# Performance work log

Measured on AMD Instinct MI355X. Metric: run time of the kernel, lower is better.

## Reference

```python
import jax, jax.numpy as jnp
from jax import lax
import numpy as np

B = 8; T = 64000
NFFT = 1024; HOP = 256
SC = 20; KS = 1024; PAD = 512
HEADS = 8; GH = 64; GO = 32
SPEC_DIM = 32 * (NFFT // 4) // 2   # 4096
NODE_DIM = SC + SPEC_DIM           # 4116
EPS = 1e-5
NEG_SLOPE = 0.2


def setup_inputs() -> dict:
    ks = jax.random.split(jax.random.key(0), 12)
    f32 = jnp.float32
    def rn(k, shp, s):
        return jax.random.normal(k, shp, dtype=f32) * s
    return {
        "x": jax.random.normal(ks[0], (B, 1, T), dtype=f32),
        "sinc_w": rn(ks[1], (SC, 1, KS), 0.03),
        "conv1_w": rn(ks[2], (32, 1, 3, 3), 0.1),
        "conv1_b": jnp.zeros((32,), f32),
        "bn1_g": jnp.ones((32,), f32),
        "bn1_b": jnp.zeros((32,), f32),
        "conv2_w": rn(ks[3], (32, 32, 3, 3), 0.06),
        "conv2_b": jnp.zeros((32,), f32),
        "bn2_g": jnp.ones((32,), f32),
        "bn2_b": jnp.zeros((32,), f32),
        "gat1_W": rn(ks[4], (NODE_DIM, HEADS * GH), 0.015),
        "gat1_asrc": rn(ks[5], (HEADS, GH), 0.1),
        "gat1_adst": rn(ks[6], (HEADS, GH), 0.1),
        "gat1_bias": jnp.zeros((HEADS * GH,), f32),
        "gat2_W": rn(ks[7], (HEADS * GH, GO), 0.04),
        "gat2_asrc": rn(ks[8], (1, GO), 0.1),
        "gat2_adst": rn(ks[9], (1, GO), 0.1),
        "gat2_bias": jnp.zeros((GO,), f32),
        "fc1_w": rn(ks[10], (GO, 128), 0.15),
        "fc1_b": jnp.zeros((128,), f32),
        "bnf_g": jnp.ones((128,), f32),
        "bnf_b": jnp.zeros((128,), f32),
        "fc2_w": rn(ks[11], (128, 2), 0.08),
        "fc2_b": jnp.zeros((2,), f32),
    }


def _bn2d_eval(z, g, b):
    # eval-mode BatchNorm2d with running_mean=0, running_var=1
    s = g / jnp.sqrt(1.0 + EPS)
    return z * s[None, :, None, None] + b[None, :, None, None]


def _conv2d(z, w, b):
    y = lax.conv_general_dilated(z, w, (1, 1), ((1, 1), (1, 1)),
                                 dimension_numbers=("NCHW", "OIHW", "NCHW"))
    return y + b[None, :, None, None]


def _gat_dense(hin, W, asrc, adst, bias, heads, fo, concat):
    # PyG GATConv on a fully-connected graph (add_self_loops=True default
    # => every node attends to all nodes including itself). Eval mode (no dropout).
    b, n, d = hin.shape
    h = jnp.einsum("bnd,dhf->bnhf", hin, W.reshape(d, heads, fo))
    s_src = jnp.einsum("bnhf,hf->bnh", h, asrc)   # alpha_j contribution
    s_dst = jnp.einsum("bnhf,hf->bnh", h, adst)   # alpha_i contribution
    e = jax.nn.leaky_relu(s_dst[:, :, None, :] + s_src[:, None, :, :], NEG_SLOPE)  # (b,i,j,h)
    a = jax.nn.softmax(e, axis=2)                 # softmax over sources j per dest i
    out = jnp.einsum("bijh,bjhf->bihf", a, h)
    out = out.reshape(b, n, heads * fo) if concat else out.mean(axis=2)
    return out + bias


def reference(x, sinc_w, conv1_w, conv1_b, bn1_g, bn1_b, conv2_w, conv2_b,
              bn2_g, bn2_b, gat1_W, gat1_asrc, gat1_adst, gat1_bias,
              gat2_W, gat2_asrc, gat2_adst, gat2_bias,
              fc1_w, fc1_b, bnf_g, bnf_b, fc2_w, fc2_b):
    b = x.shape[0]
    # --- sinc (band-pass) conv branch: conv1d k=1024, pad=512 ---
    sinc = lax.conv_general_dilated(x, sinc_w, (1,), ((PAD, PAD),),
                                    dimension_numbers=("NCH", "OIH", "NCH"))  # (b,20,T+1)
    Ls = (sinc.shape[-1] // 4) * 4
    sinc_feat = sinc[:, :, :Ls].reshape(b, SC, Ls // 4, 4).mean(-1)  # avg_pool1d(4)
    sinc_feat = jnp.transpose(sinc_feat, (0, 2, 1))                  # (b, Ls//4, 20)

    # --- STFT branch (torch.stft: center=True, reflect pad, rect window) ---
    xw = x[:, 0, :]
    xp = jnp.pad(xw, ((0, 0), (NFFT // 2, NFFT // 2)), mode="reflect")
    n_frames = 1 + T // HOP  # 251
    idx = np.arange(n_frames)[:, None] * HOP + np.arange(NFFT)
    frames = xp[:, idx]                                   # (b, 251, 1024)
    mag = jnp.abs(jnp.fft.rfft(frames, axis=-1))          # (b, 251, 513)
    logmag = jnp.log(mag + 1e-9)
    s = jnp.transpose(logmag, (0, 2, 1))[:, None]         # (b, 1, 513, 251)

    h = jax.nn.relu(_bn2d_eval(_conv2d(s, conv1_w, conv1_b), bn1_g, bn1_b))
    h = jax.nn.relu(_bn2d_eval(_conv2d(h, conv2_w, conv2_b), bn2_g, bn2_b))
    Fq = (h.shape[2] // 2) * 2
    Tt = (h.shape[3] // 2) * 2
    h = h[:, :, :Fq, :Tt].reshape(b, 32, Fq // 2, 2, Tt // 2, 2).max(axis=(3, 5))  # maxpool 2x2
    spec_feat = jnp.transpose(h, (0, 3, 1, 2)).reshape(b, -1, SPEC_DIM)  # (b, 250, 4096)

    n = min(sinc_feat.shape[1], spec_feat.shape[1])  # 250
    nodes = jnp.concatenate([sinc_feat[:, :n], spec_feat[:, :n]], axis=-1)  # (b,250,4116)

    g1 = jax.nn.relu(_gat_dense(nodes, gat1_W, gat1_asrc, gat1_adst, gat1_bias, HEADS, GH, True))
    g2 = _gat_dense(g1, gat2_W, gat2_asrc, gat2_adst, gat2_bias, 1, GO, False)
    emb = g2.mean(axis=1)  # (b, 32) graph-mean readout

    z = emb @ fc1_w + fc1_b
    z = jax.nn.relu(z * (bnf_g / jnp.sqrt(1.0 + EPS)) + bnf_b)  # eval BN1d
    out = z @ fc2_w + fc2_b
    return (out, emb)
```

## Files before the change

### kernel.cpp

```cpp
#include <hip/hip_runtime.h>
#include <hip/hip_bf16.h>
#include <math.h>

#define TB 8
#define TT 64000
#define NFRAMES 251
#define NROWS (TB*NFRAMES)
#define GROWS 2048
#define NBINS 513
#define NBPAD 576
#define NNODE 250
#define NODE_DIM 4116
#define KPAD 4128

typedef __attribute__((ext_vector_type(8))) short short8;
typedef __attribute__((ext_vector_type(4))) float floatx4;

static __device__ __forceinline__ unsigned short f2bf(float x) {
    __hip_bfloat16 h = __float2bfloat16(x);
    return *(unsigned short*)&h;
}
static __device__ __forceinline__ float bf2f(unsigned short u) {
    __hip_bfloat16 h = *(__hip_bfloat16*)&u;
    return __bfloat162float(h);
}

__global__ __launch_bounds__(256) void k_prep(
    const float* __restrict__ x, const float* __restrict__ sinc_w,
    const float* __restrict__ c2w, const float* __restrict__ g2bn,
    const float* __restrict__ c1w, const float* __restrict__ g1bn,
    const float* __restrict__ W,
    unsigned short* __restrict__ fh, unsigned short* __restrict__ fl,
    unsigned short* __restrict__ bch, unsigned short* __restrict__ bcl,
    unsigned short* __restrict__ bsh, unsigned short* __restrict__ bsl,
    unsigned short* __restrict__ wbt, unsigned short* __restrict__ Bp,
    unsigned short* __restrict__ Bc1,
    unsigned short* __restrict__ Wt, unsigned short* __restrict__ nodesb,
    unsigned short* __restrict__ h1t, unsigned short* __restrict__ h2t) {
    __shared__ unsigned short tile[64][65];
    int bi = blockIdx.x, tid = threadIdx.x;
    if (bi < 2048) {
        int idx = bi * 256 + tid;
        int row = idx >> 8, r = idx & 255;
        int b = row >> 8, j = row & 255;
        int u = j * 256 + r - 512;
        if (u < 0) u = -u;
        if (u >= TT) u = 2 * TT - 2 - u;
        float v = x[b * TT + u];
        unsigned short h = f2bf(v);
        fh[idx] = h;
        fl[idx] = f2bf(v - bf2f(h));
    } else if (bi < 2624) {
        int idx = (bi - 2048) * 256 + tid;
        int k = idx >> 8, r = idx & 255;
        float s = 0.f, c = 0.f;
        if (k < NBINS) {
            int mm = (k * r) & 1023;
            sincospif((float)mm * (1.0f / 512.0f), &s, &c);
        }
        unsigned short chv = f2bf(c), shv = f2bf(s);
        bch[idx] = chv; bcl[idx] = f2bf(c - bf2f(chv));
        bsh[idx] = shv; bsl[idx] = f2bf(s - bf2f(shv));
    } else if (bi < 3144) {
        int local = bi - 2624;
        int kt = local % 65, nt = local / 65;
        for (int idx = tid; idx < 4096; idx += 256) {
            int r = idx >> 6, c = idx & 63;
            int kp = kt * 64 + r;
            int k;
            if (kp < 20) k = kp;
            else if (kp < NODE_DIM) { int t = kp - 20; k = 20 + (t & 15) * 256 + (t >> 4); }
            else k = -1;
            float v = (k >= 0) ? W[k * 512 + nt * 64 + c] : 0.f;
            tile[r][c] = f2bf(v);
        }
        __syncthreads();
        for (int idx = tid; idx < 4096; idx += 256) {
            int nl = idx >> 6, kl = idx & 63;
            int k = kt * 64 + kl;
            if (k < KPAD)
                Wt[(size_t)(nt * 64 + nl) * KPAD + k] = tile[kl][nl];
        }
    } else if (bi < 3276) {
        int idx = (bi - 3144) * 256 + tid;
        if (idx < 32 * 1056) {
            int c = idx / 1056, m = idx - c * 1056;
            float s = 0.f;
            if (c < 20 && m < 1027) {
                #pragma unroll
                for (int d = 0; d < 4; d++) {
                    int k = m - d;
                    if (k >= 0 && k < 1024) s += sinc_w[c * 1024 + k];
                }
                s *= 0.25f;
            }
            wbt[idx] = f2bf(s);
        }
    } else if (bi < 3312) {
        int idx = (bi - 3276) * 256 + tid;
        if (idx < 9216) {
            int j = idx & 7, lane = (idx >> 3) & 63, ct = (idx >> 9) & 1, s = idx >> 10;
            int co = ct * 16 + (lane & 15);
            int ci = (lane >> 4) * 8 + j;
            float inv = rsqrtf(1.0f + 1e-5f);
            Bp[idx] = f2bf(c2w[co * 288 + ci * 9 + s] * (g2bn[co] * inv));
        }
    } else if (bi < 3508) {
        int idx = (bi - 3312) * 256 + tid;
        if (idx < 24000) {
            int row = idx / 12, c = idx - row * 12;
            nodesb[(size_t)row * KPAD + 4116 + c] = 0;
        } else if (idx < 48576) {
            int t = idx - 24000; int r = t / 6, c = t - r * 6;
            h1t[(size_t)r * 256 + 250 + c] = 0;
        } else if (idx < 50112) {
            int t = idx - 48576; int r = t / 6, c = t - r * 6;
            h2t[(size_t)r * 256 + 250 + c] = 0;
        }
    } else {
        int idx = (bi - 3508) * 256 + tid;
        if (idx < 1024) {
            int ch = idx >> 5, k = idx & 31;
            float inv = rsqrtf(1.0f + 1e-5f);
            int t; int typ;
            if (k < 8)       { t = k;      typ = 0; }
            else if (k < 16) { t = k - 8;  typ = 0; }
            else if (k < 24) { t = k - 16; typ = 1; }
            else if (k == 24 || k == 25) { t = 8; typ = 0; }
            else if (k == 26) { t = 8; typ = 1; }
            else { t = 0; typ = 2; }
            unsigned short outv = 0;
            if (typ != 2) {
                float wv = c1w[ch * 9 + t] * (g1bn[ch] * inv);
                unsigned short whi = f2bf(wv);
                outv = (typ == 0) ? whi : f2bf(wv - bf2f(whi));
            }
            Bc1[idx] = outv;
        }
    }
}

__global__ __launch_bounds__(256) void k_dftsinc(const unsigned short* __restrict__ fh,
                                                 const unsigned short* __restrict__ fl,
                                                 const unsigned short* __restrict__ ch,
                                                 const unsigned short* __restrict__ cl,
                                                 const unsigned short* __restrict__ sh,
                                                 const unsigned short* __restrict__ sl,
                                                 float* __restrict__ GTR,
                                                 float* __restrict__ GTI,
                                                 const float* __restrict__ x,
                                                 const unsigned short* __restrict__ wbt,
                                                 unsigned short* __restrict__ nodesb) {
    __shared__ __align__(16) unsigned char smem[34048];
    int tid = threadIdx.x;
    int bi = blockIdx.x;
    if (bi >= 576) {
        unsigned short* xs = (unsigned short*)smem;
        int local = bi - 576;
        int ut = local & 3, b = local >> 2;
        int base = 256 * ut - 512;
        for (int i = tid; i < 1312; i += 256) {
            int g = base + i;
            float v = (g >= 0 && g < TT) ? x[b * TT + g] : 0.f;
            xs[i] = f2bf(v);
        }
        __syncthreads();
        int w = tid >> 6, lane = tid & 63;
        int q = lane >> 4, col = lane & 15;
        floatx4 acc[2];
        acc[0] = acc[1] = (floatx4){0.f, 0.f, 0.f, 0.f};
        for (int K0 = 0; K0 < 1056; K0 += 32) {
            int off = 4 * (w * 16 + col) + K0 + q * 8;
            unsigned long long lo = *(const unsigned long long*)&xs[off];
            unsigned long long hi = *(const unsigned long long*)&xs[off + 4];
            union { unsigned long long u64[2]; short8 s8; } cv;
            cv.u64[0] = lo; cv.u64[1] = hi;
            short8 af = cv.s8;
            #pragma unroll
            for (int ni = 0; ni < 2; ni++) {
                short8 bf = *(const short8*)(wbt + (size_t)(ni * 16 + col) * 1056 + K0 + q * 8);
                acc[ni] = __builtin_amdgcn_mfma_f32_16x16x32_bf16(af, bf, acc[ni], 0, 0, 0);
            }
        }
        #pragma unroll
        for (int ni = 0; ni < 2; ni++)
            #pragma unroll
            for (int rr = 0; rr < 4; rr++) {
                int u = ut * 64 + w * 16 + q * 4 + rr;
                int c = ni * 16 + col;
                if (u < NNODE && c < 20)
                    nodesb[(size_t)(b * NNODE + u) * KPAD + c] = f2bf(acc[ni][rr]);
            }
        return;
    }
    unsigned short* Ah  = (unsigned short*)smem;
    unsigned short* Al  = (unsigned short*)(smem + 2560);
    unsigned short* Bch = (unsigned short*)(smem + 5120);
    unsigned short* Bcl = (unsigned short*)(smem + 10240);
    unsigned short* Bsh = (unsigned short*)(smem + 15360);
    unsigned short* Bsl = (unsigned short*)(smem + 20480);
    float* TR = (float*)(smem + 25600);
    int N0 = (bi % 9) * 64, M0 = (bi / 9) * 32;
    int br = tid >> 2, bc = (tid & 3) * 8;
    size_t boff = (size_t)(N0 + br) * 256 + bc;
    int ar = (tid & 127) >> 2, ac = (tid & 3) * 8;
    size_t aoff = (size_t)(M0 + ar) * 256 + ac;
    bool loA = tid < 128;
    int w = tid >> 6, lane = tid & 63;
    int q = lane >> 4, col = lane & 15;
    int mb = (w >> 1) * 16, nb = (w & 1) * 32;
    floatx4 aR[2], aI[2];
    aR[0] = aR[1] = aI[0] = aI[1] = (floatx4){0.f, 0.f, 0.f, 0.f};

    for (int K0 = 0; K0 < 256; K0 += 32) {
        if (loA) *(short8*)&Ah[ar * 40 + ac] = *(const short8*)(fh + aoff + K0);
        else     *(short8*)&Al[ar * 40 + ac] = *(const short8*)(fl + aoff + K0);
        *(short8*)&Bch[br * 40 + bc] = *(const short8*)(ch + boff + K0);
        *(short8*)&Bcl[br * 40 + bc] = *(const short8*)(cl + boff + K0);
        *(short8*)&Bsh[br * 40 + bc] = *(const short8*)(sh + boff + K0);
        *(short8*)&Bsl[br * 40 + bc] = *(const short8*)(sl + boff + K0);
        __syncthreads();
        short8 ahv = *(const short8*)&Ah[(mb + col) * 40 + q * 8];
        short8 alv = *(const short8*)&Al[(mb + col) * 40 + q * 8];
        #pragma unroll
        for (int ni = 0; ni < 2; ni++) {
            short8 chv = *(const short8*)&Bch[(nb + ni * 16 + col) * 40 + q * 8];
            short8 clv = *(const short8*)&Bcl[(nb + ni * 16 + col) * 40 + q * 8];
            short8 shv = *(const short8*)&Bsh[(nb + ni * 16 + col) * 40 + q * 8];
            short8 slv = *(const short8*)&Bsl[(nb + ni * 16 + col) * 40 + q * 8];
            aR[ni] = __builtin_amdgcn_mfma_f32_16x16x32_bf16(ahv, chv, aR[ni], 0, 0, 0);
            aR[ni] = __builtin_amdgcn_mfma_f32_16x16x32_bf16(ahv, clv, aR[ni], 0, 0, 0);
            aR[ni] = __builtin_amdgcn_mfma_f32_16x16x32_bf16(alv, chv, aR[ni], 0, 0, 0);
            aI[ni] = __builtin_amdgcn_mfma_f32_16x16x32_bf16(ahv, shv, aI[ni], 0, 0, 0);
            aI[ni] = __builtin_amdgcn_mfma_f32_16x16x32_bf16(ahv, slv, aI[ni], 0, 0, 0);
            aI[ni] = __builtin_amdgcn_mfma_f32_16x16x32_bf16(alv, shv, aI[ni], 0, 0, 0);
        }
        __syncthreads();
    }
    int bin_l = tid >> 2, ms = (tid & 3) * 8;
    #pragma unroll
    for (int ni = 0; ni < 2; ni++)
        #pragma unroll
        for (int rr = 0; rr < 4; rr++)
            TR[(nb + ni * 16 + col) * 33 + mb + q * 4 + rr] = aR[ni][rr];
    __syncthreads();
    {
        float* dst = GTR + (size_t)(N0 + bin_l) * 2048 + M0 + ms;
        #pragma unroll
        for (int j = 0; j < 8; j++) dst[j] = TR[bin_l * 33 + ms + j];
    }
    __syncthreads();
    #pragma unroll
    for (int ni = 0; ni < 2; ni++)
        #pragma unroll
        for (int rr = 0; rr < 4; rr++)
            TR[(nb + ni * 16 + col) * 33 + mb + q * 4 + rr] = aI[ni][rr];
    __syncthreads();
    {
        float* dst = GTI + (size_t)(N0 + bin_l) * 2048 + M0 + ms;
        #pragma unroll
        for (int j = 0; j < 8; j++) dst[j] = TR[bin_l * 33 + ms + j];
    }
}

#define O1STR 40
__global__ __launch_bounds__(256) void k_conv2f(const float* __restrict__ GTR,
                                                const float* __restrict__ GTI,
                                                const unsigned short* __restrict__ Bc1,
                                                const float* __restrict__ c1b,
                                                const float* __restrict__ g1bn,
                                                const float* __restrict__ b1bn,
                                                const unsigned short* __restrict__ Bp,
                                                const float* __restrict__ c2b,
                                                const float* __restrict__ g2bn,
                                                const float* __restrict__ b2bn,
                                                unsigned short* __restrict__ nodesb) {
    __shared__ __align__(16) unsigned short o1s[18 * 18 * O1STR];
    __shared__ float S0s[20][20];
    __shared__ float b1s[32];
    __shared__ float b2s[32];
    int tid = threadIdx.x;
    int b = blockIdx.z;
    int F0 = blockIdx.y * 8;
    int T0 = blockIdx.x * 8;
    float inv = rsqrtf(1.0f + 1e-5f);
    if (tid < 32) {
        b1s[tid] = c1b[tid] * (g1bn[tid] * inv) + b1bn[tid];
        b2s[tid] = c2b[tid] * (g2bn[tid] * inv) + b2bn[tid];
    }
    for (int i = tid; i < 400; i += 256) {
        int r = i / 20, c = i - r * 20;
        int bin = 2 * F0 - 2 + r, fr = 2 * T0 - 2 + c;
        float v = 0.f;
        if (bin >= 0 && bin < 513 && fr >= 0 && fr < 251) {
            size_t base = (size_t)bin * 2048 + b * 256 + fr;
            float gr0 = GTR[base], gr1 = GTR[base + 1], gr2 = GTR[base + 2], gr3 = GTR[base + 3];
            float gs0 = GTI[base], gs1 = GTI[base + 1], gs2 = GTI[base + 2], gs3 = GTI[base + 3];
            float fre, fim;
            switch (bin & 3) {
                case 0: fre = gr0 + gr1 + gr2 + gr3; fim = gs0 + gs1 + gs2 + gs3; break;
                case 1: fre = gr0 - gs1 - gr2 + gs3; fim = gs0 + gr1 - gs2 - gr3; break;
                case 2: fre = gr0 - gr1 + gr2 - gr3; fim = gs0 - gs1 + gs2 - gs3; break;
                default: fre = gr0 + gs1 - gr2 - gs3; fim = gs0 - gr1 - gs2 + gr3; break;
            }
            v = logf(sqrtf(fmaf(fre, fre, fim * fim)) + 1e-9f);
        }
        S0s[r][c] = v;
    }
    __syncthreads();

    int lane = tid & 63, w = tid >> 6;
    int q = lane >> 4, col = lane & 15;

    {
        short8 bfr0 = *(const short8*)(Bc1 + (size_t)col * 32 + q * 8);
        short8 bfr1 = *(const short8*)(Bc1 + (size_t)(16 + col) * 32 + q * 8);
        for (int mt = w; mt < 21; mt += 4) {
            int p = mt * 16 + col;
            int pc = p < 324 ? p : 0;
            int pr = (pc * 228) >> 12;
            int pt = pc - pr * 18;
            float tv[9];
            #pragma unroll
            for (int di = 0; di < 3; di++)
                #pragma unroll
                for (int dj = 0; dj < 3; dj++)
                    tv[di * 3 + dj] = S0s[pr + di][pt + dj];
            unsigned short hu[9], lu[9];
            #pragma unroll
            for (int i = 0; i < 9; i++) {
                hu[i] = f2bf(tv[i]);
                lu[i] = f2bf(tv[i] - bf2f(hu[i]));
            }
            short8 af;
            if (q == 1) {
                af[0] = lu[0]; af[1] = lu[1]; af[2] = lu[2]; af[3] = lu[3];
                af[4] = lu[4]; af[5] = lu[5]; af[6] = lu[6]; af[7] = lu[7];
            } else if (q == 3) {
                af[0] = hu[8]; af[1] = lu[8]; af[2] = hu[8]; af[3] = 0;
                af[4] = 0; af[5] = 0; af[6] = 0; af[7] = 0;
            } else {
                af[0] = hu[0]; af[1] = hu[1]; af[2] = hu[2]; af[3] = hu[3];
                af[4] = hu[4]; af[5] = hu[5]; af[6] = hu[6]; af[7] = hu[7];
            }
            floatx4 c0 = (floatx4){0.f, 0.f, 0.f, 0.f};
            floatx4 c1 = (floatx4){0.f, 0.f, 0.f, 0.f};
            c0 = __builtin_amdgcn_mfma_f32_16x16x32_bf16(af, bfr0, c0, 0, 0, 0);
            c1 = __builtin_amdgcn_mfma_f32_16x16x32_bf16(af, bfr1, c1, 0, 0, 0);
            #pragma unroll
            for (int rr2 = 0; rr2 < 4; rr2++) {
                int pp = mt * 16 + q * 4 + rr2;
                if (pp < 324) {
                    int qr = (pp * 228) >> 12, qt = pp - qr * 18;
                    int r1 = 2 * F0 - 1 + qr, t1 = 2 * T0 - 1 + qt;
                    bool valid = (r1 >= 0 && r1 < 513 && t1 >= 0 && t1 < 251);
                    float v0 = fmaxf(c0[rr2] + b1s[col], 0.f);
                    float v1 = fmaxf(c1[rr2] + b1s[16 + col], 0.f);
                    o1s[pp * O1STR + col]      = valid ? f2bf(v0) : (unsigned short)0;
                    o1s[pp * O1STR + 16 + col] = valid ? f2bf(v1) : (unsigned short)0;
                }
            }
        }
    }
    __syncthreads();

    floatx4 acc[4][2];
    #pragma unroll
    for (int rt = 0; rt < 4; rt++)
        #pragma unroll
        for (int ct = 0; ct < 2; ct++)
            acc[rt][ct] = (floatx4){0.f, 0.f, 0.f, 0.f};

    #pragma unroll
    for (int s = 0; s < 9; s++) {
        const int di = s / 3, dj = s % 3;
        short8 bf0 = *(const short8*)&Bp[(s * 2 + 0) * 512 + lane * 8];
        short8 bf1 = *(const short8*)&Bp[(s * 2 + 1) * 512 + lane * 8];
        #pragma unroll
        for (int rt = 0; rt < 4; rt++) {
            short8 af = *(const short8*)&o1s[((w * 4 + rt + di) * 18 + (col + dj)) * O1STR + q * 8];
            acc[rt][0] = __builtin_amdgcn_mfma_f32_16x16x32_bf16(af, bf0, acc[rt][0], 0, 0, 0);
            acc[rt][1] = __builtin_amdgcn_mfma_f32_16x16x32_bf16(af, bf1, acc[rt][1], 0, 0, 0);
        }
    }
    __syncthreads();

    unsigned short* nb = o1s;
    #pragma unroll
    for (int ct = 0; ct < 2; ct++) {
        float bb = b2s[ct * 16 + col];
        #pragma unroll
        for (int fp2 = 0; fp2 < 2; fp2++)
            #pragma unroll
            for (int tc2 = 0; tc2 < 2; tc2++) {
                float m0 = fmaxf(
                    fmaxf(acc[2 * fp2][ct][2 * tc2], acc[2 * fp2][ct][2 * tc2 + 1]),
                    fmaxf(acc[2 * fp2 + 1][ct][2 * tc2], acc[2 * fp2 + 1][ct][2 * tc2 + 1]));
                float v = fmaxf(m0 + bb, 0.f);
                int nl = (2 * q + tc2) * 2 + ct;
                int fl = 2 * w + fp2;
                nb[nl * 136 + fl * 16 + col] = f2bf(v);
            }
    }
    __syncthreads();

    int nl = tid >> 4, part = tid & 15;
    int node_g = 2 * T0 + nl;
    if (node_g < NNODE) {
        unsigned short* dst = nodesb + (size_t)(b * NNODE + node_g) * KPAD + 20 + F0 * 16 + part * 8;
        *(short8*)(dst) = *(const short8*)&nb[nl * 136 + part * 8];
    }
}

__global__ __launch_bounds__(256) void k_gat1s(const unsigned short* __restrict__ A,
                                               const unsigned short* __restrict__ Bt,
                                               float* __restrict__ hpart) {
    __shared__ __align__(16) unsigned short As[64 * 40];
    __shared__ __align__(16) unsigned short Bs[64 * 40];
    int tid = threadIdx.x;
    int N0 = blockIdx.x * 64, M0 = blockIdx.y * 64;
    int kc = blockIdx.z;
    int ks = (kc == 0) ? 0 : (33 + 32 * (kc - 1));
    int ke = 33 + 32 * kc;
    if (kc == 0) ke = 33;
    int sr = tid >> 2, sc = (tid & 3) * 8;
    int w = tid >> 6, lane = tid & 63;
    int q = lane >> 4, col = lane & 15;
    int mb = (w >> 1) * 32, nb = (w & 1) * 32;
    floatx4 acc[2][2];
    acc[0][0] = acc[0][1] = acc[1][0] = acc[1][1] = (floatx4){0.f, 0.f, 0.f, 0.f};
    short8 z8 = {0, 0, 0, 0, 0, 0, 0, 0};
    int mA = M0 + sr;
    bool mv = mA < 2000;
    const unsigned short* pa = A + (size_t)mA * KPAD + sc;
    const unsigned short* pb = Bt + (size_t)(N0 + sr) * KPAD + sc;

    for (int kk = ks; kk < ke; kk++) {
        int K0 = kk * 32;
        short8 va = mv ? *(const short8*)(pa + K0) : z8;
        short8 vb = *(const short8*)(pb + K0);
        *(short8*)&As[sr * 40 + sc] = va;
        *(short8*)&Bs[sr * 40 + sc] = vb;
        __syncthreads();
        short8 a0 = *(const short8*)&As[(mb + col) * 40 + q * 8];
        short8 a1 = *(const short8*)&As[(mb + 16 + col) * 40 + q * 8];
        short8 b0 = *(const short8*)&Bs[(nb + col) * 40 + q * 8];
        short8 b1 = *(const short8*)&Bs[(nb + 16 + col) * 40 + q * 8];
        acc[0][0] = __builtin_amdgcn_mfma_f32_16x16x32_bf16(a0, b0, acc[0][0], 0, 0, 0);
        acc[0][1] = __builtin_amdgcn_mfma_f32_16x16x32_bf16(a0, b1, acc[0][1], 0, 0, 0);
        acc[1][0] = __builtin_amdgcn_mfma_f32_16x16x32_bf16(a1, b0, acc[1][0], 0, 0, 0);
        acc[1][1] = __builtin_amdgcn_mfma_f32_16x16x32_bf16(a1, b1, acc[1][1], 0, 0, 0);
        __syncthreads();
    }
    float* out = hpart + (size_t)kc * 1024000;
    #pragma unroll
    for (int mi = 0; mi < 2; mi++)
        #pragma unroll
        for (int ni = 0; ni < 2; ni++)
            #pragma unroll
            for (int rr = 0; rr < 4; rr++) {
                int m = M0 + mb + mi * 16 + q * 4 + rr;
                if (m < 2000)
                    out[m * 512 + N0 + nb + ni * 16 + col] = acc[mi][ni][rr];
            }
}

__global__ __launch_bounds__(256) void k_hred(const float* __restrict__ hpart,
                                              const float* __restrict__ asrc,
                                              const float* __restrict__ adst,
                                              unsigned short* __restrict__ h1t,
                                              float* __restrict__ ssrc,
                                              float* __restrict__ sdst) {
    int m = blockIdx.x;
    int tid = threadIdx.x;
    int n1 = tid, n2 = tid + 256;
    size_t base = (size_t)m * 512;
    float s1 = hpart[base + n1] + hpart[base + n1 + 1024000] +
               hpart[base + n1 + 2048000] + hpart[base + n1 + 3072000];
    float s2 = hpart[base + n2] + hpart[base + n2 + 1024000] +
               hpart[base + n2 + 2048000] + hpart[base + n2 + 3072000];
    int bb = m / NNODE, j = m - bb * NNODE;
    int hh1 = n1 >> 6, f1 = n1 & 63;
    int hh2 = n2 >> 6, f2 = n2 & 63;
    h1t[((size_t)((bb * 8 + hh1) * 64 + f1)) * 256 + j] = f2bf(s1);
    h1t[((size_t)((bb * 8 + hh2) * 64 + f2)) * 256 + j] = f2bf(s2);
    float ps1 = s1 * asrc[n1], pd1 = s1 * adst[n1];
    float ps2 = s2 * asrc[n2], pd2 = s2 * adst[n2];
    for (int off = 32; off > 0; off >>= 1) {
        ps1 += __shfl_down(ps1, off); pd1 += __shfl_down(pd1, off);
        ps2 += __shfl_down(ps2, off); pd2 += __shfl_down(pd2, off);
    }
    int lane = tid & 63, w = tid >> 6;
    if (lane == 0) {
        ssrc[m * 8 + w] = ps1;     sdst[m * 8 + w] = pd1;
        ssrc[m * 8 + 4 + w] = ps2; sdst[m * 8 + 4 + w] = pd2;
    }
}

#define PSTR 264
__global__ __launch_bounds__(256) void k_att1(const float* __restrict__ ssrc,
                                              const float* __restrict__ sdst,
                                              const unsigned short* __restrict__ h1t,
                                              const float* __restrict__ bias,
                                              float* __restrict__ g1) {
    __shared__ __align__(16) unsigned short Ps[128 * PSTR];
    __shared__ float ss[NNODE];
    __shared__ float red[4];
    int mhalf = blockIdx.x, bh = blockIdx.y;
    int b = bh >> 3, h = bh & 7;
    int tid = threadIdx.x;
    for (int j = tid; j < NNODE; j += 256) ss[j] = ssrc[(b * NNODE + j) * 8 + h];
    __syncthreads();
    float mv = (tid < NNODE) ? ss[tid] : -1e30f;
    for (int off = 32; off > 0; off >>= 1) mv = fmaxf(mv, __shfl_down(mv, off));
    if ((tid & 63) == 0) red[tid >> 6] = mv;
    __syncthreads();
    float smaxv = fmaxf(fmaxf(red[0], red[1]), fmaxf(red[2], red[3]));
    if (tid < 128) {
        unsigned short* row = Ps + tid * PSTR;
        int row_g = mhalf * 128 + tid;
        short8 z8 = {0, 0, 0, 0, 0, 0, 0, 0};
        if (row_g >= NNODE) {
            #pragma unroll
            for (int j = 0; j < 256; j += 8) *(short8*)(row + j) = z8;
        } else {
            float d = sdst[(b * NNODE + row_g) * 8 + h];
            float e0 = d + smaxv;
            float mx = e0 > 0.f ? e0 : 0.2f * e0;
            float den = 0.f;
            for (int j = 0; j < NNODE; j++) {
                float e = d + ss[j];
                e = e > 0.f ? e : 0.2f * e;
                den += __expf(e - mx);
            }
            float rden = 1.f / den;
            for (int j0 = 0; j0 < 256; j0 += 8) {
                unsigned short wv[8];
                #pragma unroll
                for (int jj = 0; jj < 8; jj++) {
                    int j = j0 + jj;
                    float wt = 0.f;
                    if (j < NNODE) {
                        float e = d + ss[j];
                        e = e > 0.f ? e : 0.2f * e;
                        wt = __expf(e - mx) * rden;
                    }
                    wv[jj] = f2bf(wt);
                }
                *(short8*)(row + j0) = *(const short8*)wv;
            }
        }
    }
    __syncthreads();
    int w = tid >> 6, lane = tid & 63;
    int q = lane >> 4, col = lane & 15;
    const unsigned short* Hb = h1t + (size_t)bh * 16384;
    floatx4 acc[2][4];
    #pragma unroll
    for (int mi = 0; mi < 2; mi++)
        #pragma unroll
        for (int ni = 0; ni < 4; ni++)
            acc[mi][ni] = (floatx4){0.f, 0.f, 0.f, 0.f};
    for (int k0 = 0; k0 < 256; k0 += 32) {
        short8 af[2], bf[4];
        #pragma unroll
        for (int mi = 0; mi < 2; mi++)
            af[mi] = *(const short8*)&Ps[((w * 2 + mi) * 16 + col) * PSTR + k0 + q * 8];
        #pragma unroll
        for (int ni = 0; ni < 4; ni++)
            bf[ni] = *(const short8*)(Hb + (size_t)(ni * 16 + col) * 256 + k0 + q * 8);
        #pragma unroll
        for (int mi = 0; mi < 2; mi++)
            #pragma unroll
            for (int ni = 0; ni < 4; ni++)
                acc[mi][ni] = __builtin_amdgcn_mfma_f32_16x16x32_bf16(af[mi], bf[ni], acc[mi][ni], 0, 0, 0);
    }
    #pragma unroll
    for (int mi = 0; mi < 2; mi++)
        #pragma unroll
        for (int ni = 0; ni < 4; ni++)
            #pragma unroll
            for (int rr = 0; rr < 4; rr++) {
                int i = mhalf * 128 + (w * 2 + mi) * 16 + q * 4 + rr;
                int f = ni * 16 + col;
                if (i < NNODE)
                    g1[(b * NNODE + i) * 512 + h * 64 + f] =
                        fmaxf(acc[mi][ni][rr] + bias[h * 64 + f], 0.f);
            }
}

__global__ __launch_bounds__(256) void k_h2(const float* __restrict__ g1,
                                            const float* __restrict__ W2,
                                            const float* __restrict__ a2src,
                                            const float* __restrict__ a2dst,
                                            unsigned short* __restrict__ h2t,
                                            float* __restrict__ s2src,
                                            float* __restrict__ s2dst) {
    int row = blockIdx.x * 4 + (threadIdx.x >> 6);
    if (row >= 2000) return;
    int lane = threadIdx.x & 63;
    int o = lane & 31, half = lane >> 5;
    const float* gr = &g1[row * 512 + half * 256];
    float acc = 0.f;
    for (int k = 0; k < 256; k++) acc = fmaf(gr[k], W2[(half * 256 + k) * 32 + o], acc);
    acc += __shfl_down(acc, 32);
    float ps = acc * a2src[o], pd = acc * a2dst[o];
    for (int off = 16; off > 0; off >>= 1) {
        ps += __shfl_down(ps, off, 32);
        pd += __shfl_down(pd, off, 32);
    }
    if (lane == 0) { s2src[row] = ps; s2dst[row] = pd; }
    if (lane < 32) {
        int b = row / NNODE, j = row - b * NNODE;
        h2t[((size_t)(b * 32 + o)) * 256 + j] = f2bf(acc);
    }
}

__global__ __launch_bounds__(256) void k_att2(const float* __restrict__ s2src,
                                              const float* __restrict__ s2dst,
                                              const unsigned short* __restrict__ h2t,
                                              const float* __restrict__ bias2,
                                              float* __restrict__ g2) {
    __shared__ __align__(16) unsigned short Ps[256 * PSTR];
    __shared__ float ss[NNODE];
    __shared__ float red[4];
    int b = blockIdx.x;
    int tid = threadIdx.x;
    for (int j = tid; j < NNODE; j += 256) ss[j] = s2src[b * NNODE + j];
    __syncthreads();
    float mv = (tid < NNODE) ? ss[tid] : -1e30f;
    for (int off = 32; off > 0; off >>= 1) mv = fmaxf(mv, __shfl_down(mv, off));
    if ((tid & 63) == 0) red[tid >> 6] = mv;
    __syncthreads();
    float smaxv = fmaxf(fmaxf(red[0], red[1]), fmaxf(red[2], red[3]));
    {
        unsigned short* row = Ps + tid * PSTR;
        short8 z8 = {0, 0, 0, 0, 0, 0, 0, 0};
        if (tid >= NNODE) {
            #pragma unroll
            for (int j = 0; j < 256; j += 8) *(short8*)(row + j) = z8;
        } else {
            float d = s2dst[b * NNODE + tid];
            float e0 = d + smaxv;
            float mx = e0 > 0.f ? e0 : 0.2f * e0;
            float den = 0.f;
            for (int j = 0; j < NNODE; j++) {
                float e = d + ss[j];
                e = e > 0.f ? e : 0.2f * e;
                den += __expf(e - mx);
            }
            float rden = 1.f / den;
            for (int j0 = 0; j0 < 256; j0 += 8) {
                unsigned short wv[8];
                #pragma unroll
                for (int jj = 0; jj < 8; jj++) {
                    int j = j0 + jj;
                    float wt = 0.f;
                    if (j < NNODE) {
                        float e = d + ss[j];
                        e = e > 0.f ? e : 0.2f * e;
                        wt = __expf(e - mx) * rden;
                    }
                    wv[jj] = f2bf(wt);
                }
                *(short8*)(row + j0) = *(const short8*)wv;
            }
        }
    }
    __syncthreads();
    int w = tid >> 6, lane = tid & 63;
    int q = lane >> 4, col = lane & 15;
    const unsigned short* Hb = h2t + (size_t)b * 8192;
    floatx4 acc[4][2];
    #pragma unroll
    for (int mi = 0; mi < 4; mi++)
        #pragma unroll
        for (int ni = 0; ni < 2; ni++)
            acc[mi][ni] = (floatx4){0.f, 0.f, 0.f, 0.f};
    for (int k0 = 0; k0 < 256; k0 += 32) {
        short8 af[4], bf[2];
        #pragma unroll
        for (int mi = 0; mi < 4; mi++)
            af[mi] = *(const short8*)&Ps[((w * 4 + mi) * 16 + col) * PSTR + k0 + q * 8];
        #pragma unroll
        for (int ni = 0; ni < 2; ni++)
            bf[ni] = *(const short8*)(Hb + (size_t)(ni * 16 + col) * 256 + k0 + q * 8);
        #pragma unroll
        for (int mi = 0; mi < 4; mi++)
            #pragma unroll
            for (int ni = 0; ni < 2; ni++)
                acc[mi][ni] = __builtin_amdgcn_mfma_f32_16x16x32_bf16(af[mi], bf[ni], acc[mi][ni], 0, 0, 0);
    }
    #pragma unroll
    for (int mi = 0; mi < 4; mi++)
        #pragma unroll
        for (int ni = 0; ni < 2; ni++)
            #pragma unroll
            for (int rr = 0; rr < 4; rr++) {
                int i = (w * 4 + mi) * 16 + q * 4 + rr;
                int f = ni * 16 + col;
                if (i < NNODE)
                    g2[(b * NNODE + i) * 32 + f] = acc[mi][ni][rr] + bias2[f];
            }
}

__global__ __launch_bounds__(256) void k_fc(const float* __restrict__ g2,
                                            const float* __restrict__ fc1w,
                                            const float* __restrict__ fc1b,
                                            const float* __restrict__ bnfg,
                                            const float* __restrict__ bnfb,
                                            const float* __restrict__ fc2w,
                                            const float* __restrict__ fc2b,
                                            float* __restrict__ dout) {
    __shared__ float es[256];
    __shared__ float zs[1024];
    int tid = threadIdx.x;
    {
        int b = tid >> 5, f = tid & 31;
        float s = 0.f;
        #pragma unroll 5
        for (int i = 0; i < NNODE; i++) s += g2[((size_t)(b * NNODE + i)) * 32 + f];
        s *= (1.0f / 250.0f);
        es[tid] = s;
        dout[16 + tid] = s;
    }
    __syncthreads();
    float inv = rsqrtf(1.0f + 1e-5f);
    #pragma unroll
    for (int rep = 0; rep < 4; rep++) {
        int idx = tid + rep * 256;
        int b = idx >> 7, j = idx & 127;
        float a = fc1b[j];
        #pragma unroll
        for (int k = 0; k < 32; k++) a = fmaf(es[b * 32 + k], fc1w[k * 128 + j], a);
        a = a * (bnfg[j] * inv) + bnfb[j];
        zs[idx] = fmaxf(a, 0.f);
    }
    __syncthreads();
    if (tid < 16) {
        int b = tid >> 1, o = tid & 1;
        float a = fc2b[o];
        for (int k = 0; k < 128; k++) a = fmaf(zs[b * 128 + k], fc2w[k * 2 + o], a);
        dout[b * 2 + o] = a;
    }
}

extern "C" void kernel_launch(void* const* d_in, const int* in_sizes, int n_in,
                              void* d_out, int out_size, void* d_ws, size_t ws_size,
                              hipStream_t stream) {
    (void)in_sizes; (void)n_in; (void)out_size; (void)ws_size;
    const float* x       = (const float*)d_in[0];
    const float* sinc_w  = (const float*)d_in[1];
    const float* conv1_w = (const float*)d_in[2];
    const float* conv1_b = (const float*)d_in[3];
    const float* bn1_g   = (const float*)d_in[4];
    const float* bn1_b   = (const float*)d_in[5];
    const float* conv2_w = (const float*)d_in[6];
    const float* conv2_b = (const float*)d_in[7];
    const float* bn2_g   = (const float*)d_in[8];
    const float* bn2_b   = (const float*)d_in[9];
    const float* gat1_W  = (const float*)d_in[10];
    const float* gat1_as = (const float*)d_in[11];
    const float* gat1_ad = (const float*)d_in[12];
    const float* gat1_bi = (const float*)d_in[13];
    const float* gat2_W  = (const float*)d_in[14];
    const float* gat2_as = (const float*)d_in[15];
    const float* gat2_ad = (const float*)d_in[16];
    const float* gat2_bi = (const float*)d_in[17];
    const float* fc1_w   = (const float*)d_in[18];
    const float* fc1_b   = (const float*)d_in[19];
    const float* bnf_g   = (const float*)d_in[20];
    const float* bnf_b   = (const float*)d_in[21];
    const float* fc2_w   = (const float*)d_in[22];
    const float* fc2_b   = (const float*)d_in[23];
    float* dout = (float*)d_out;

    unsigned short* fh  = (unsigned short*)d_ws;
    unsigned short* fl  = fh + (size_t)GROWS * 256;
    unsigned short* bch = fl + (size_t)GROWS * 256;
    unsigned short* bcl = bch + (size_t)NBPAD * 256;
    unsigned short* bsh = bcl + (size_t)NBPAD * 256;
    unsigned short* bsl = bsh + (size_t)NBPAD * 256;
    float* GTR = (float*)(bsl + (size_t)NBPAD * 256);
    float* GTI = GTR + (size_t)GROWS * NBPAD;
    float* S0  = GTI + (size_t)GROWS * NBPAD;
    unsigned short* wbt = (unsigned short*)(S0 + 1030104);
    unsigned short* bpk = wbt + 32 * 1056;
    unsigned short* Bc1 = bpk + 9216;
    unsigned short* Wt  = Bc1 + 1024;
    unsigned short* nodesb = Wt + (size_t)512 * KPAD;
    unsigned short* Pn  = nodesb + (size_t)2000 * KPAD;
    unsigned short* h1t = Pn + (size_t)64 * 256 * 256;
    unsigned short* h2t = h1t + (size_t)64 * 64 * 256;
    unsigned short* P2n = h2t + (size_t)8 * 32 * 256;
    float* hpart = (float*)(P2n + (size_t)8 * 256 * 256);
    float* ssrc1 = hpart + 4 * 1024000;
    float* sdst1 = ssrc1 + 16000;
    float* g1    = sdst1 + 16000;
    float* s2src = g1 + 1024000;
    float* s2dst = s2src + 2000;
    float* g2    = s2dst + 2000;

    hipLaunchKernelGGL(k_prep, dim3(3512), dim3(256), 0, stream,
                       x, sinc_w, conv2_w, bn2_g, conv1_w, bn1_g, gat1_W,
                       fh, fl, bch, bcl, bsh, bsl, wbt, bpk, Bc1, Wt, nodesb, h1t, h2t);
    hipLaunchKernelGGL(k_dftsinc, dim3(608), dim3(256), 0, stream,
                       fh, fl, bch, bcl, bsh, bsl, GTR, GTI, x, wbt, nodesb);
    hipLaunchKernelGGL(k_conv2f, dim3(16, 32, 8), dim3(256), 0, stream,
                       GTR, GTI, Bc1, conv1_b, bn1_g, bn1_b, bpk, conv2_b, bn2_g, bn2_b, nodesb);
    hipLaunchKernelGGL(k_gat1s, dim3(8, 32, 4), dim3(256), 0, stream, nodesb, Wt, hpart);
    hipLaunchKernelGGL(k_hred, dim3(2000), dim3(256), 0, stream,
                       hpart, gat1_as, gat1_ad, h1t, ssrc1, sdst1);
    hipLaunchKernelGGL(k_att1, dim3(2, 64), dim3(256), 0, stream,
                       ssrc1, sdst1, h1t, gat1_bi, g1);
    hipLaunchKernelGGL(k_h2, dim3(500), dim3(256), 0, stream,
                       g1, gat2_W, gat2_as, gat2_ad, h2t, s2src, s2dst);
    hipLaunchKernelGGL(k_att2, dim3(8), dim3(256), 0, stream,
                       s2src, s2dst, h2t, gat2_bi, g2);
    hipLaunchKernelGGL(k_fc, dim3(1), dim3(256), 0, stream,
                       g2, fc1_w, fc1_b, bnf_g, bnf_b, fc2_w, fc2_b, dout);
}
```

Measured before the change: 313.2 us.

## Fuse split-K reduction into GAT1 attention and fold FC head into GAT2

Removes the k_hred kernel. Each k_att1 block now sums the four split-K partials for its batch/head slice, converts to bf16 into shared memory, and computes the source/destination attention scores in place. This drops the h1t and score round-trips through global memory. It also removes the k_fc launch: each k_att2 block reduces its graph mean in shared memory and runs the small FC head for its batch, cutting two launches. The cost is that each k_att1 block (two per batch-head) redundantly re-reduces the same partials, giving less parallelism than 2000 blocks for that reduction. Shared memory per block also grows.

```diff
diff --git a/kernel.cpp b/kernel.cpp
--- a/kernel.cpp
+++ b/kernel.cpp
@@ -36,7 +36,7 @@
     unsigned short* __restrict__ wbt, unsigned short* __restrict__ Bp,
     unsigned short* __restrict__ Bc1,
     unsigned short* __restrict__ Wt, unsigned short* __restrict__ nodesb,
-    unsigned short* __restrict__ h1t, unsigned short* __restrict__ h2t) {
+    unsigned short* __restrict__ h2t) {
     __shared__ unsigned short tile[64][65];
     int bi = blockIdx.x, tid = threadIdx.x;
     if (bi < 2048) {
@@ -110,11 +110,8 @@
         if (idx < 24000) {
             int row = idx / 12, c = idx - row * 12;
             nodesb[(size_t)row * KPAD + 4116 + c] = 0;
-        } else if (idx < 48576) {
+        } else if (idx < 25536) {
             int t = idx - 24000; int r = t / 6, c = t - r * 6;
-            h1t[(size_t)r * 256 + 250 + c] = 0;
-        } else if (idx < 50112) {
-            int t = idx - 48576; int r = t / 6, c = t - r * 6;
             h2t[(size_t)r * 256 + 250 + c] = 0;
         }
     } else {
@@ -465,53 +462,43 @@
             }
 }
 
-__global__ __launch_bounds__(256) void k_hred(const float* __restrict__ hpart,
+#define PSTR 264
+__global__ __launch_bounds__(256) void k_att1(const float* __restrict__ hpart,
                                               const float* __restrict__ asrc,
                                               const float* __restrict__ adst,
-                                              unsigned short* __restrict__ h1t,
-                                              float* __restrict__ ssrc,
-                                              float* __restrict__ sdst) {
-    int m = blockIdx.x;
-    int tid = threadIdx.x;
-    int n1 = tid, n2 = tid + 256;
-    size_t base = (size_t)m * 512;
-    float s1 = hpart[base + n1] + hpart[base + n1 + 1024000] +
-               hpart[base + n1 + 2048000] + hpart[base + n1 + 3072000];
-    float s2 = hpart[base + n2] + hpart[base + n2 + 1024000] +
-               hpart[base + n2 + 2048000] + hpart[base + n2 + 3072000];
-    int bb = m / NNODE, j = m - bb * NNODE;
-    int hh1 = n1 >> 6, f1 = n1 & 63;
-    int hh2 = n2 >> 6, f2 = n2 & 63;
-    h1t[((size_t)((bb * 8 + hh1) * 64 + f1)) * 256 + j] = f2bf(s1);
-    h1t[((size_t)((bb * 8 + hh2) * 64 + f2)) * 256 + j] = f2bf(s2);
-    float ps1 = s1 * asrc[n1], pd1 = s1 * adst[n1];
-    float ps2 = s2 * asrc[n2], pd2 = s2 * adst[n2];
-    for (int off = 32; off > 0; off >>= 1) {
-        ps1 += __shfl_down(ps1, off); pd1 += __shfl_down(pd1, off);
-        ps2 += __shfl_down(ps2, off); pd2 += __shfl_down(pd2, off);
-    }
-    int lane = tid & 63, w = tid >> 6;
-    if (lane == 0) {
-        ssrc[m * 8 + w] = ps1;     sdst[m * 8 + w] = pd1;
-        ssrc[m * 8 + 4 + w] = ps2; sdst[m * 8 + 4 + w] = pd2;
-    }
-}
-
-#define PSTR 264
-__global__ __launch_bounds__(256) void k_att1(const float* __restrict__ ssrc,
-                                              const float* __restrict__ sdst,
-                                              const unsigned short* __restrict__ h1t,
                                               const float* __restrict__ bias,
                                               float* __restrict__ g1) {
     __shared__ __align__(16) unsigned short Ps[128 * PSTR];
-    __shared__ float ss[NNODE];
+    __shared__ __align__(16) unsigned short hL[64 * PSTR];
+    __shared__ float ssA[NNODE];
+    __shared__ float sdA[NNODE];
     __shared__ float red[4];
     int mhalf = blockIdx.x, bh = blockIdx.y;
     int b = bh >> 3, h = bh & 7;
     int tid = threadIdx.x;
-    for (int j = tid; j < NNODE; j += 256) ss[j] = ssrc[(b * NNODE + j) * 8 + h];
-    __syncthreads();
-    float mv = (tid < NNODE) ? ss[tid] : -1e30f;
+    int lane = tid & 63, w = tid >> 6;
+    {
+        float av = asrc[h * 64 + lane];
+        float dv = adst[h * 64 + lane];
+        for (int j = w; j < 256; j += 4) {
+            if (j < NNODE) {
+                size_t base = ((size_t)(b * NNODE + j)) * 512 + h * 64 + lane;
+                float s = hpart[base] + hpart[base + 1024000] +
+                          hpart[base + 2048000] + hpart[base + 3072000];
+                hL[lane * PSTR + j] = f2bf(s);
+                float ps = s * av, pd = s * dv;
+                for (int off = 32; off > 0; off >>= 1) {
+                    ps += __shfl_down(ps, off);
+                    pd += __shfl_down(pd, off);
+                }
+                if (lane == 0) { ssA[j] = ps; sdA[j] = pd; }
+            } else {
+                hL[lane * PSTR + j] = 0;
+            }
+        }
+    }
+    __syncthreads();
+    float mv = (tid < NNODE) ? ssA[tid] : -1e30f;
     for (int off = 32; off > 0; off >>= 1) mv = fmaxf(mv, __shfl_down(mv, off));
     if ((tid & 63) == 0) red[tid >> 6] = mv;
     __syncthreads();
@@ -524,12 +511,12 @@
             #pragma unroll
             for (int j = 0; j < 256; j += 8) *(short8*)(row + j) = z8;
         } else {
-            float d = sdst[(b * NNODE + row_g) * 8 + h];
+            float d = sdA[row_g];
             float e0 = d + smaxv;
             float mx = e0 > 0.f ? e0 : 0.2f * e0;
             float den = 0.f;
             for (int j = 0; j < NNODE; j++) {
-                float e = d + ss[j];
+                float e = d + ssA[j];
                 e = e > 0.f ? e : 0.2f * e;
                 den += __expf(e - mx);
             }
@@ -541,7 +528,7 @@
                     int j = j0 + jj;
                     float wt = 0.f;
                     if (j < NNODE) {
-                        float e = d + ss[j];
+                        float e = d + ssA[j];
                         e = e > 0.f ? e : 0.2f * e;
                         wt = __expf(e - mx) * rden;
                     }
@@ -552,9 +539,7 @@
         }
     }
     __syncthreads();
-    int w = tid >> 6, lane = tid & 63;
     int q = lane >> 4, col = lane & 15;
-    const unsigned short* Hb = h1t + (size_t)bh * 16384;
     floatx4 acc[2][4];
     #pragma unroll
     for (int mi = 0; mi < 2; mi++)
@@ -568,7 +553,7 @@
             af[mi] = *(const short8*)&Ps[((w * 2 + mi) * 16 + col) * PSTR + k0 + q * 8];
         #pragma unroll
         for (int ni = 0; ni < 4; ni++)
-            bf[ni] = *(const short8*)(Hb + (size_t)(ni * 16 + col) * 256 + k0 + q * 8);
+            bf[ni] = *(const short8*)&hL[(ni * 16 + col) * PSTR + k0 + q * 8];
         #pragma unroll
         for (int mi = 0; mi < 2; mi++)
             #pragma unroll
@@ -620,10 +605,18 @@
                                               const float* __restrict__ s2dst,
                                               const unsigned short* __restrict__ h2t,
                                               const float* __restrict__ bias2,
-                                              float* __restrict__ g2) {
+                                              const float* __restrict__ fc1w,
+                                              const float* __restrict__ fc1b,
+                                              const float* __restrict__ bnfg,
+                                              const float* __restrict__ bnfb,
+                                              const float* __restrict__ fc2w,
+                                              const float* __restrict__ fc2b,
+                                              float* __restrict__ dout) {
     __shared__ __align__(16) unsigned short Ps[256 * PSTR];
     __shared__ float ss[NNODE];
     __shared__ float red[4];
+    __shared__ float es2[32];
+    __shared__ float zs2[128];
     int b = blockIdx.x;
     int tid = threadIdx.x;
     for (int j = tid; j < NNODE; j += 256) ss[j] = s2src[b * NNODE + j];
@@ -691,6 +684,8 @@
             for (int ni = 0; ni < 2; ni++)
                 acc[mi][ni] = __builtin_amdgcn_mfma_f32_16x16x32_bf16(af[mi], bf[ni], acc[mi][ni], 0, 0, 0);
     }
+    __syncthreads();
+    float* gf = (float*)Ps;
     #pragma unroll
     for (int mi = 0; mi < 4; mi++)
         #pragma unroll
@@ -699,48 +694,32 @@
             for (int rr = 0; rr < 4; rr++) {
                 int i = (w * 4 + mi) * 16 + q * 4 + rr;
                 int f = ni * 16 + col;
-                if (i < NNODE)
-                    g2[(b * NNODE + i) * 32 + f] = acc[mi][ni][rr] + bias2[f];
-            }
-}
-
-__global__ __launch_bounds__(256) void k_fc(const float* __restrict__ g2,
-                                            const float* __restrict__ fc1w,
-                                            const float* __restrict__ fc1b,
-                                            const float* __restrict__ bnfg,
-                                            const float* __restrict__ bnfb,
-                                            const float* __restrict__ fc2w,
-                                            const float* __restrict__ fc2b,
-                                            float* __restrict__ dout) {
-    __shared__ float es[256];
-    __shared__ float zs[1024];
-    int tid = threadIdx.x;
-    {
-        int b = tid >> 5, f = tid & 31;
+                gf[i * 33 + f] = acc[mi][ni][rr] + bias2[f];
+            }
+    __syncthreads();
+    if (tid < 32) {
+        int f = tid;
         float s = 0.f;
-        #pragma unroll 5
-        for (int i = 0; i < NNODE; i++) s += g2[((size_t)(b * NNODE + i)) * 32 + f];
+        for (int i = 0; i < NNODE; i++) s += gf[i * 33 + f];
         s *= (1.0f / 250.0f);
-        es[tid] = s;
-        dout[16 + tid] = s;
+        es2[f] = s;
+        dout[16 + b * 32 + f] = s;
     }
     __syncthreads();
     float inv = rsqrtf(1.0f + 1e-5f);
-    #pragma unroll
-    for (int rep = 0; rep < 4; rep++) {
-        int idx = tid + rep * 256;
-        int b = idx >> 7, j = idx & 127;
+    if (tid < 128) {
+        int j = tid;
         float a = fc1b[j];
         #pragma unroll
-        for (int k = 0; k < 32; k++) a = fmaf(es[b * 32 + k], fc1w[k * 128 + j], a);
+        for (int k = 0; k < 32; k++) a = fmaf(es2[k], fc1w[k * 128 + j], a);
         a = a * (bnfg[j] * inv) + bnfb[j];
-        zs[idx] = fmaxf(a, 0.f);
-    }
-    __syncthreads();
-    if (tid < 16) {
-        int b = tid >> 1, o = tid & 1;
+        zs2[j] = fmaxf(a, 0.f);
+    }
+    __syncthreads();
+    if (tid < 2) {
+        int o = tid;
         float a = fc2b[o];
-        for (int k = 0; k < 128; k++) a = fmaf(zs[b * 128 + k], fc2w[k * 2 + o], a);
+        for (int k = 0; k < 128; k++) a = fmaf(zs2[k], fc2w[k * 2 + o], a);
         dout[b * 2 + o] = a;
     }
 }
@@ -799,24 +778,20 @@
     float* g1    = sdst1 + 16000;
     float* s2src = g1 + 1024000;
     float* s2dst = s2src + 2000;
-    float* g2    = s2dst + 2000;
 
     hipLaunchKernelGGL(k_prep, dim3(3512), dim3(256), 0, stream,
                        x, sinc_w, conv2_w, bn2_g, conv1_w, bn1_g, gat1_W,
-                       fh, fl, bch, bcl, bsh, bsl, wbt, bpk, Bc1, Wt, nodesb, h1t, h2t);
+                       fh, fl, bch, bcl, bsh, bsl, wbt, bpk, Bc1, Wt, nodesb, h2t);
     hipLaunchKernelGGL(k_dftsinc, dim3(608), dim3(256), 0, stream,
                        fh, fl, bch, bcl, bsh, bsl, GTR, GTI, x, wbt, nodesb);
     hipLaunchKernelGGL(k_conv2f, dim3(16, 32, 8), dim3(256), 0, stream,
                        GTR, GTI, Bc1, conv1_b, bn1_g, bn1_b, bpk, conv2_b, bn2_g, bn2_b, nodesb);
     hipLaunchKernelGGL(k_gat1s, dim3(8, 32, 4), dim3(256), 0, stream, nodesb, Wt, hpart);
-    hipLaunchKernelGGL(k_hred, dim3(2000), dim3(256), 0, stream,
-                       hpart, gat1_as, gat1_ad, h1t, ssrc1, sdst1);
     hipLaunchKernelGGL(k_att1, dim3(2, 64), dim3(256), 0, stream,
-                       ssrc1, sdst1, h1t, gat1_bi, g1);
+                       hpart, gat1_as, gat1_ad, gat1_bi, g1);
     hipLaunchKernelGGL(k_h2, dim3(500), dim3(256), 0, stream,
                        g1, gat2_W, gat2_as, gat2_ad, h2t, s2src, s2dst);
     hipLaunchKernelGGL(k_att2, dim3(8), dim3(256), 0, stream,
-                       s2src, s2dst, h2t, gat2_bi, g2);
-    hipLaunchKernelGGL(k_fc, dim3(1), dim3(256), 0, stream,
-                       g2, fc1_w, fc1_b, bnf_g, bnf_b, fc2_w, fc2_b, dout);
-}
+                       s2src, s2dst, h2t, gat2_bi,
+                       fc1_w, fc1_b, bnf_g, bnf_b, fc2_w, fc2_b, dout);
+}
```

Result: no change. 310.9 us (-0.7%).
